# Performance work log

Hardware: AMD Instinct MI355X
Metric: run time of the kernel (lower is better)

Reference implementation:

```python
import jax, jax.numpy as jnp
import numpy as np

B, N, C = 8, 1024, 768
H, D = 12, 64
SCALE = D ** -0.5
EPS = 1e-5

def layernorm(x, g, b):
    mu = jnp.mean(x, axis=-1, keepdims=True)
    var = jnp.var(x, axis=-1, keepdims=True)
    return (x - mu) * jax.lax.rsqrt(var + EPS) * g + b

def setup_inputs() -> dict:
    key = jax.random.key(0)
    ks = jax.random.split(key, 5)
    return {
        "x": jax.random.normal(ks[0], (B, N, C), jnp.float32),
        "qkv_w": jax.random.normal(ks[1], (3 * C, C), jnp.float32) * 0.02,
        "qkv_b": jax.random.normal(ks[2], (3 * C,), jnp.float32) * 0.02,
        "qn_g": jnp.ones((D,), jnp.float32),
        "qn_b": jnp.zeros((D,), jnp.float32),
        "kn_g": jnp.ones((D,), jnp.float32),
        "kn_b": jnp.zeros((D,), jnp.float32),
        "proj_w": jax.random.normal(ks[3], (C, C), jnp.float32) * 0.02,
        "proj_b": jnp.zeros((C,), jnp.float32),
    }

def reference(x, qkv_w, qkv_b, qn_g, qn_b, kn_g, kn_b, proj_w, proj_b):
    # qkv projection: [B,N,3C] -> [3,B,H,N,D]
    qkv = jnp.einsum('bnc,oc->bno', x, qkv_w) + qkv_b
    qkv = qkv.reshape(B, N, 3, H, D).transpose(2, 0, 3, 1, 4)
    q, k, v = qkv[0], qkv[1], qkv[2]
    q = layernorm(q, qn_g, qn_b) * SCALE
    k = layernorm(k, kn_g, kn_b)
    # explicit attention matrix [B,H,N,N] (module stores it)
    attn = jax.nn.softmax(jnp.einsum('bhqd,bhkd->bhqk', q, k), axis=-1)
    out = jnp.einsum('bhqk,bhkd->bhqd', attn, v)
    out = out.transpose(0, 2, 1, 3).reshape(B, N, C)
    out = jnp.einsum('bnc,oc->bno', out, proj_w) + proj_b
    return out
```

## Files before the change

### kernel.cpp

```cpp
#include <hip/hip_runtime.h>
#include <cstdint>

#define Bz 8
#define Nn 1024
#define Cc 768
#define Hh 12
#define Dd 64
#define C3 2304
#define BN 8192

constexpr float EPS = 1e-5f;
constexpr float QSCALE = 0.125f * 1.44269504088896340736f;

typedef __attribute__((ext_vector_type(8))) short bf16x8;
typedef _Float16 f16x8 __attribute__((ext_vector_type(8)));
typedef __attribute__((ext_vector_type(4))) float f32x4;
typedef __attribute__((ext_vector_type(16))) float f32x16;

__device__ __forceinline__ short f2b(float f) {
    union { float f; unsigned u; } x; x.f = f;
    unsigned r = x.u + 0x7FFFu + ((x.u >> 16) & 1u);
    return (short)(r >> 16);
}
__device__ __forceinline__ unsigned cvtpk(float a, float b) {
    unsigned r;
    asm("v_cvt_pk_bf16_f32 %0, %1, %2" : "=v"(r) : "v"(a), "v"(b));
    return r;
}

__device__ __forceinline__ f32x4 MFMAH(f16x8 a, f16x8 b, f32x4 c) {
    return __builtin_amdgcn_mfma_f32_16x16x32_f16(a, b, c, 0, 0, 0);
}
__device__ __forceinline__ f32x16 MFMA32(bf16x8 a, bf16x8 b, f32x16 c) {
    return __builtin_amdgcn_mfma_f32_32x32x16_bf16(a, b, c, 0, 0, 0);
}
__device__ __forceinline__ f16x8 ldf16(const _Float16* p) { return *(const f16x8*)p; }
__device__ __forceinline__ void gld16(const void* g, void* l) {
    __builtin_amdgcn_global_load_lds((const __attribute__((address_space(1))) unsigned int*)g,
                                     (__attribute__((address_space(3))) unsigned int*)(l),
                                     16, 0, 0);
}

__global__ __launch_bounds__(256) void cvt_all(
    const float* __restrict__ x, const float* __restrict__ wq, const float* __restrict__ wp,
    _Float16* __restrict__ xh, _Float16* __restrict__ wqh, _Float16* __restrict__ wph)
{
    const int n1 = BN * Cc / 8, n2 = n1 + C3 * Cc / 8, n3 = n2 + Cc * Cc / 8;
    int i = blockIdx.x * 256 + threadIdx.x;
    const float* s; _Float16* d; int off;
    if (i < n1)      { s = x;  d = xh;  off = i; }
    else if (i < n2) { s = wq; d = wqh; off = i - n1; }
    else if (i < n3) { s = wp; d = wph; off = i - n2; }
    else return;
    float4 a = *(const float4*)(s + (size_t)off * 8);
    float4 b = *(const float4*)(s + (size_t)off * 8 + 4);
    f16x8 o;
    o[0] = (_Float16)a.x; o[1] = (_Float16)a.y; o[2] = (_Float16)a.z; o[3] = (_Float16)a.w;
    o[4] = (_Float16)b.x; o[5] = (_Float16)b.y; o[6] = (_Float16)b.z; o[7] = (_Float16)b.w;
    *(f16x8*)(d + (size_t)off * 8) = o;
}

template<int EPI>
__global__ __launch_bounds__(256, 4) void gemm_f16(
    const _Float16* __restrict__ A,
    const _Float16* __restrict__ W,
    const float* __restrict__ bias,
    float* __restrict__ Out,
    short* __restrict__ qp, short* __restrict__ kp, short* __restrict__ vp,
    const float* __restrict__ qg, const float* __restrict__ qb,
    const float* __restrict__ kg, const float* __restrict__ kb,
    int nx)
{
    __shared__ _Float16 As[128 * 64];
    __shared__ _Float16 Bs[128 * 64];
    const int tid = threadIdx.x;
    const int lane = tid & 63;
    const int w = tid >> 6;
    const int wr = w >> 1, wc = w & 1;
    const int l15 = lane & 15, l4 = lane >> 4;
    const int lr = lane >> 3;
    const int lslot = lane & 7;

    const int chunk = gridDim.x >> 3;
    const int wg = (blockIdx.x & 7) * chunk + (blockIdx.x >> 3);
    const int by = wg / nx;
    int bx = wg % nx;
    if (by & 1) bx = nx - 1 - bx;
    const int m0 = by * 128;
    const int n0 = bx * 128;

    auto stage = [&](int kt) {
        const int k0 = kt * 64;
#pragma unroll
        for (int j = 0; j < 8; ++j) {
            int i = w * 8 + j;
            int isA = (i < 16);
            int ib = isA ? i : i - 16;
            int row = ib * 8 + lr;
            int gslot = lslot ^ (row & 7);
            const _Float16* src = (isA ? A + (size_t)(m0 + row) * 768
                                       : W + (size_t)(n0 + row) * 768) + k0 + gslot * 8;
            _Float16* dst = (isA ? As : Bs) + ib * 512;
            gld16(src, dst);
        }
    };

    f32x4 acc[4][4];
#pragma unroll
    for (int mi = 0; mi < 4; ++mi)
#pragma unroll
        for (int ni = 0; ni < 4; ++ni) { acc[mi][ni][0]=0.f; acc[mi][ni][1]=0.f; acc[mi][ni][2]=0.f; acc[mi][ni][3]=0.f; }

    stage(0);
    for (int kt = 0; kt < 12; ++kt) {
        __syncthreads();
#pragma unroll
        for (int ks = 0; ks < 2; ++ks) {
            f16x8 af[4], bfr[4];
#pragma unroll
            for (int mi = 0; mi < 4; ++mi) {
                int row = wr * 64 + mi * 16 + l15;
                int slot = (ks * 4 + l4) ^ (row & 7);
                af[mi] = ldf16(&As[row * 64 + slot * 8]);
            }
#pragma unroll
            for (int ni = 0; ni < 4; ++ni) {
                int row = wc * 64 + ni * 16 + l15;
                int slot = (ks * 4 + l4) ^ (row & 7);
                bfr[ni] = ldf16(&Bs[row * 64 + slot * 8]);
            }
#pragma unroll
            for (int mi = 0; mi < 4; ++mi)
#pragma unroll
                for (int ni = 0; ni < 4; ++ni)
                    acc[mi][ni] = MFMAH(af[mi], bfr[ni], acc[mi][ni]);
        }
        __syncthreads();
        if (kt < 11) stage(kt + 1);
    }

    if (EPI == 0) {
#pragma unroll
        for (int mi = 0; mi < 4; ++mi)
#pragma unroll
            for (int r = 0; r < 4; ++r) {
                int row = m0 + wr * 64 + mi * 16 + l4 * 4 + r;
#pragma unroll
                for (int ni = 0; ni < 4; ++ni) {
                    int col = n0 + wc * 64 + ni * 16 + l15;
                    Out[(size_t)row * Cc + col] = acc[mi][ni][r] + bias[col];
                }
            }
    } else {
        const int ncol0 = n0 + wc * 64;
        const int type = ncol0 / Cc;
        const int h = (ncol0 % Cc) >> 6;
        const float* gptr = (type == 0) ? qg : kg;
        const float* bptr = (type == 0) ? qb : kb;
        float biasv[4], gv[4], bv[4];
#pragma unroll
        for (int ni = 0; ni < 4; ++ni) {
            int d = ni * 16 + l15;
            biasv[ni] = bias[ncol0 + d];
            if (type < 2) { gv[ni] = gptr[d]; bv[ni] = bptr[d]; }
        }
        short* plane = (type == 0) ? qp : (type == 1) ? kp : vp;
#pragma unroll
        for (int mi = 0; mi < 4; ++mi)
#pragma unroll
            for (int r = 0; r < 4; ++r) {
                float v[4];
#pragma unroll
                for (int ni = 0; ni < 4; ++ni) v[ni] = acc[mi][ni][r] + biasv[ni];
                int row = m0 + wr * 64 + mi * 16 + l4 * 4 + r;
                size_t base = ((size_t)row * Hh + h) * 64;
                if (type < 2) {
                    float s = v[0] + v[1] + v[2] + v[3];
#pragma unroll
                    for (int off = 1; off < 16; off <<= 1) s += __shfl_xor(s, off);
                    float mu = s * (1.0f / 64.0f);
                    float s2 = 0.f;
#pragma unroll
                    for (int ni = 0; ni < 4; ++ni) { float dv = v[ni] - mu; s2 += dv * dv; }
#pragma unroll
                    for (int off = 1; off < 16; off <<= 1) s2 += __shfl_xor(s2, off);
                    float inv = rsqrtf(s2 * (1.0f / 64.0f) + EPS);
#pragma unroll
                    for (int ni = 0; ni < 4; ++ni) {
                        float rr = (v[ni] - mu) * inv * gv[ni] + bv[ni];
                        if (type == 0) rr *= QSCALE;
                        plane[base + ni * 16 + l15] = f2b(rr);
                    }
                } else {
#pragma unroll
                    for (int ni = 0; ni < 4; ++ni)
                        plane[base + ni * 16 + l15] = f2b(v[ni]);
                }
            }
    }
}

__global__ __launch_bounds__(128, 3) void flash_attn_mfma(
    const short* __restrict__ qp, const short* __restrict__ kp, const short* __restrict__ vp,
    _Float16* __restrict__ att)
{
    __shared__ short kls[64 * 64];
    __shared__ short vtl[2][64 * 64];
    const int tid = threadIdx.x;
    const int lane = tid & 63;
    const int w = tid >> 6;
    const int l31 = lane & 31;
    const int hi = lane >> 5;
    const int lr = lane >> 3;
    const int lslot = lane & 7;
    const int bid = (blockIdx.x & 7) * 192 + (blockIdx.x >> 3);
    const int qt = bid & 15;
    const int bh = bid >> 4;
    const int h = bh % Hh;
    const int b = bh / Hh;
    const int q0 = qt * 64;
    const size_t hbase = ((size_t)b * Nn * Hh + h) * 64;
    const int n0v = (tid & 31) * 2, d0v = (tid >> 5) * 16;
    const int khalf = n0v & 31;
    const int t2v = n0v >> 5;
    const int ksig = khalf ^ ((((khalf >> 2) ^ (khalf >> 3)) & 1) * 12);
    const int colv = t2v * 32 + ksig;

    bf16x8 qf[4];
    {
        const short* qsrc = qp + hbase + (size_t)(q0 + w * 32 + l31) * 768 + hi * 8;
#pragma unroll
        for (int ds = 0; ds < 4; ++ds)
            qf[ds] = *(const bf16x8*)(qsrc + ds * 16);
    }

    auto kstage = [&](int kt) {
#pragma unroll
        for (int j = 0; j < 4; ++j) {
            int i = w * 4 + j;
            int row = i * 8 + lr;
            gld16(kp + hbase + (size_t)(kt * 64 + row) * 768 + (lslot ^ lr) * 8,
                  &kls[i * 512]);
        }
    };
    auto vload = [&](int kt, bf16x8* va) {
        const short* s0 = vp + hbase + (size_t)(kt * 64 + n0v) * 768 + d0v;
        va[0] = *(const bf16x8*)s0;
        va[1] = *(const bf16x8*)(s0 + 8);
        va[2] = *(const bf16x8*)(s0 + 768);
        va[3] = *(const bf16x8*)(s0 + 768 + 8);
    };
    auto vcommit = [&](int buf, const bf16x8* va) {
#pragma unroll
        for (int g = 0; g < 2; ++g)
#pragma unroll
            for (int j = 0; j < 8; ++j) {
                int d = d0v + g * 8 + j;
                int fv = (d ^ (d >> 3)) & 7;
                unsigned pku = (unsigned short)va[g][j] | ((unsigned)(unsigned short)va[g + 2][j] << 16);
                *(unsigned*)&vtl[buf][d * 64 + (((colv >> 3) ^ fv) << 3) + (colv & 7)] = pku;
            }
    };

    kstage(0);
    {
        bf16x8 va[4];
        vload(0, va);
        vcommit(0, va);
    }
    __syncthreads();

    f32x16 o0, o1;
#pragma unroll
    for (int i = 0; i < 16; ++i) { o0[i] = 0.f; o1[i] = 0.f; }
    float lrun = 0.f;

    for (int kt = 0; kt < 16; ++kt) {
        const int cur = kt & 1, nxt = cur ^ 1;
        bf16x8 va[4];
        if (kt < 15) vload(kt + 1, va);
        f32x16 st0, st1;
#pragma unroll
        for (int i = 0; i < 16; ++i) { st0[i] = 0.f; st1[i] = 0.f; }
        __builtin_amdgcn_s_setprio(1);
#pragma unroll
        for (int ds = 0; ds < 4; ++ds) {
            bf16x8 kf0 = *(const bf16x8*)&kls[l31 * 64 + (((ds * 2 + hi) ^ (l31 & 7)) << 3)];
            bf16x8 kf1 = *(const bf16x8*)&kls[(32 + l31) * 64 + (((ds * 2 + hi) ^ ((32 + l31) & 7)) << 3)];
            st0 = MFMA32(kf0, qf[ds], st0);
            st1 = MFMA32(kf1, qf[ds], st1);
        }
        __builtin_amdgcn_s_setprio(0);
        __builtin_amdgcn_s_barrier();
        if (kt < 15) kstage(kt + 1);
        unsigned pk[2][8];
#pragma unroll
        for (int i = 0; i < 16; ++i) st0[i] = exp2f(st0[i]);
#pragma unroll
        for (int i = 0; i < 16; ++i) st1[i] = exp2f(st1[i]);
        {
            float a0 = 0.f, a1 = 0.f;
#pragma unroll
            for (int i = 0; i < 16; ++i) { a0 += st0[i]; a1 += st1[i]; }
            lrun += a0 + a1;
        }
#pragma unroll
        for (int i = 0; i < 8; ++i) { pk[0][i] = cvtpk(st0[2 * i], st0[2 * i + 1]);
                                      pk[1][i] = cvtpk(st1[2 * i], st1[2 * i + 1]); }
        __builtin_amdgcn_s_setprio(1);
#pragma unroll
        for (int t2 = 0; t2 < 2; ++t2)
#pragma unroll
            for (int c = 0; c < 2; ++c) {
                union { bf16x8 v; unsigned u[4]; } a;
                a.u[0] = pk[t2][c * 4 + 0]; a.u[1] = pk[t2][c * 4 + 1];
                a.u[2] = pk[t2][c * 4 + 2]; a.u[3] = pk[t2][c * 4 + 3];
#pragma unroll
                for (int nt = 0; nt < 2; ++nt) {
                    int r = nt * 32 + l31;
                    int fv = (r ^ (r >> 3)) & 7;
                    bf16x8 vf = *(const bf16x8*)&vtl[cur][r * 64 + (((t2 * 4 + c * 2 + hi) ^ fv) << 3)];
                    if (nt == 0) o0 = MFMA32(a.v, vf, o0);
                    else         o1 = MFMA32(a.v, vf, o1);
                }
            }
        __builtin_amdgcn_s_setprio(0);
        if (kt < 15) vcommit(nxt, va);
        __syncthreads();
    }

    lrun += __shfl_xor(lrun, 32);
    float linv = 1.0f / lrun;
#pragma unroll
    for (int r = 0; r < 16; ++r) {
        int qr = (r & 3) + 8 * (r >> 2) + 4 * hi;
        float invr = __shfl(linv, qr);
        int row = q0 + w * 32 + qr;
        _Float16* dst = att + (size_t)(b * Nn + row) * Cc + h * 64 + l31;
        dst[0]  = (_Float16)(o0[r] * invr);
        dst[32] = (_Float16)(o1[r] * invr);
    }
}

extern "C" void kernel_launch(void* const* d_in, const int* in_sizes, int n_in,
                              void* d_out, int out_size, void* d_ws, size_t ws_size,
                              hipStream_t stream)
{
    const float* x      = (const float*)d_in[0];
    const float* qkv_w  = (const float*)d_in[1];
    const float* qkv_b  = (const float*)d_in[2];
    const float* qn_g   = (const float*)d_in[3];
    const float* qn_b   = (const float*)d_in[4];
    const float* kn_g   = (const float*)d_in[5];
    const float* kn_b   = (const float*)d_in[6];
    const float* proj_w = (const float*)d_in[7];
    const float* proj_b = (const float*)d_in[8];
    float* out = (float*)d_out;

    char* ws = (char*)d_ws;
    short*    qp  = (short*)(ws);
    short*    kp  = (short*)(ws + 12582912);
    short*    vp  = (short*)(ws + 25165824);
    _Float16* att = (_Float16*)(ws + 37748736);
    _Float16* xh  = (_Float16*)(ws + 50331648);
    _Float16* wqh = (_Float16*)(ws + 62914560);
    _Float16* wph = (_Float16*)(ws + 66453504);

    {
        const int n3 = BN * Cc / 8 + C3 * Cc / 8 + Cc * Cc / 8;
        cvt_all<<<(n3 + 255) / 256, 256, 0, stream>>>(x, qkv_w, proj_w, xh, wqh, wph);
    }
    gemm_f16<1><<<(BN / 128) * (C3 / 128), 256, 0, stream>>>(
        xh, wqh, qkv_b, nullptr, qp, kp, vp, qn_g, qn_b, kn_g, kn_b, C3 / 128);
    flash_attn_mfma<<<Bz * Hh * 16, 128, 0, stream>>>(qp, kp, vp, att);
    gemm_f16<0><<<(BN / 128) * (Cc / 128), 256, 0, stream>>>(
        att, wph, proj_b, out, nullptr, nullptr, nullptr, nullptr, nullptr, nullptr, nullptr, Cc / 128);
}
```

Before: 126.8 us.

## Double query tile per attention block and double-buffer K in shared memory

Each attention block now handles 128 query rows (64 per wave, two 32-row halves) instead of 64, so every K/V tile loaded into LDS is reused across twice as many queries and the grid halves. The K tile gets a second LDS buffer so the next tile is prefetched at the top of the iteration, which removes the mid-loop barrier. The V transpose packing uses a byte-permute intrinsic instead of shift/or. The cost is more accumulator registers and lower occupancy (launch bound 2 instead of 3), with fewer blocks to spread across CUs.

```diff
diff --git a/kernel.cpp b/kernel.cpp
--- a/kernel.cpp
+++ b/kernel.cpp
@@ -200,11 +200,11 @@
     }
 }
 
-__global__ __launch_bounds__(128, 3) void flash_attn_mfma(
+__global__ __launch_bounds__(128, 2) void flash_attn_mfma(
     const short* __restrict__ qp, const short* __restrict__ kp, const short* __restrict__ vp,
     _Float16* __restrict__ att)
 {
-    __shared__ short kls[64 * 64];
+    __shared__ short kls[2][64 * 64];
     __shared__ short vtl[2][64 * 64];
     const int tid = threadIdx.x;
     const int lane = tid & 63;
@@ -213,12 +213,12 @@
     const int hi = lane >> 5;
     const int lr = lane >> 3;
     const int lslot = lane & 7;
-    const int bid = (blockIdx.x & 7) * 192 + (blockIdx.x >> 3);
-    const int qt = bid & 15;
-    const int bh = bid >> 4;
+    const int bid = (blockIdx.x & 7) * 96 + (blockIdx.x >> 3);
+    const int qt = bid & 7;
+    const int bh = bid >> 3;
     const int h = bh % Hh;
     const int b = bh / Hh;
-    const int q0 = qt * 64;
+    const int q0 = qt * 128;
     const size_t hbase = ((size_t)b * Nn * Hh + h) * 64;
     const int n0v = (tid & 31) * 2, d0v = (tid >> 5) * 16;
     const int khalf = n0v & 31;
@@ -226,21 +226,22 @@
     const int ksig = khalf ^ ((((khalf >> 2) ^ (khalf >> 3)) & 1) * 12);
     const int colv = t2v * 32 + ksig;
 
-    bf16x8 qf[4];
-    {
-        const short* qsrc = qp + hbase + (size_t)(q0 + w * 32 + l31) * 768 + hi * 8;
+    bf16x8 qf[2][4];
+#pragma unroll
+    for (int qh = 0; qh < 2; ++qh) {
+        const short* qsrc = qp + hbase + (size_t)(q0 + w * 64 + qh * 32 + l31) * 768 + hi * 8;
 #pragma unroll
         for (int ds = 0; ds < 4; ++ds)
-            qf[ds] = *(const bf16x8*)(qsrc + ds * 16);
-    }
-
-    auto kstage = [&](int kt) {
+            qf[qh][ds] = *(const bf16x8*)(qsrc + ds * 16);
+    }
+
+    auto kstage = [&](int kt, int buf) {
 #pragma unroll
         for (int j = 0; j < 4; ++j) {
             int i = w * 4 + j;
             int row = i * 8 + lr;
             gld16(kp + hbase + (size_t)(kt * 64 + row) * 768 + (lslot ^ lr) * 8,
-                  &kls[i * 512]);
+                  &kls[buf][i * 512]);
         }
     };
     auto vload = [&](int kt, bf16x8* va) {
@@ -251,18 +252,22 @@
         va[3] = *(const bf16x8*)(s0 + 768 + 8);
     };
     auto vcommit = [&](int buf, const bf16x8* va) {
-#pragma unroll
-        for (int g = 0; g < 2; ++g)
+        union { bf16x8 v; unsigned u[4]; } a0, a1;
+#pragma unroll
+        for (int g = 0; g < 2; ++g) {
+            a0.v = va[g]; a1.v = va[g + 2];
 #pragma unroll
             for (int j = 0; j < 8; ++j) {
                 int d = d0v + g * 8 + j;
                 int fv = (d ^ (d >> 3)) & 7;
-                unsigned pku = (unsigned short)va[g][j] | ((unsigned)(unsigned short)va[g + 2][j] << 16);
+                unsigned pku = __builtin_amdgcn_perm(a1.u[j >> 1], a0.u[j >> 1],
+                                                     (j & 1) ? 0x07060302u : 0x05040100u);
                 *(unsigned*)&vtl[buf][d * 64 + (((colv >> 3) ^ fv) << 3) + (colv & 7)] = pku;
             }
+        }
     };
 
-    kstage(0);
+    kstage(0, 0);
     {
         bf16x8 va[4];
         vload(0, va);
@@ -270,58 +275,73 @@
     }
     __syncthreads();
 
-    f32x16 o0, o1;
-#pragma unroll
-    for (int i = 0; i < 16; ++i) { o0[i] = 0.f; o1[i] = 0.f; }
-    float lrun = 0.f;
+    f32x16 o[2][2];
+#pragma unroll
+    for (int qh = 0; qh < 2; ++qh)
+#pragma unroll
+        for (int nt = 0; nt < 2; ++nt)
+#pragma unroll
+            for (int i = 0; i < 16; ++i) o[qh][nt][i] = 0.f;
+    float lrun[2] = {0.f, 0.f};
 
     for (int kt = 0; kt < 16; ++kt) {
         const int cur = kt & 1, nxt = cur ^ 1;
         bf16x8 va[4];
-        if (kt < 15) vload(kt + 1, va);
-        f32x16 st0, st1;
-#pragma unroll
-        for (int i = 0; i < 16; ++i) { st0[i] = 0.f; st1[i] = 0.f; }
+        if (kt < 15) {
+            vload(kt + 1, va);
+            kstage(kt + 1, nxt);
+        }
+        unsigned pk[2][2][8];
+#pragma unroll
+        for (int t2 = 0; t2 < 2; ++t2) {
+            const int row = t2 * 32 + l31;
+            const int rsw = row & 7;
+            bf16x8 kf[4];
+#pragma unroll
+            for (int ds = 0; ds < 4; ++ds)
+                kf[ds] = *(const bf16x8*)&kls[cur][row * 64 + (((ds * 2 + hi) ^ rsw) << 3)];
+            f32x16 st0, st1;
+#pragma unroll
+            for (int i = 0; i < 16; ++i) { st0[i] = 0.f; st1[i] = 0.f; }
+            __builtin_amdgcn_s_setprio(1);
+#pragma unroll
+            for (int ds = 0; ds < 4; ++ds) {
+                st0 = MFMA32(kf[ds], qf[0][ds], st0);
+                st1 = MFMA32(kf[ds], qf[1][ds], st1);
+            }
+            __builtin_amdgcn_s_setprio(0);
+#pragma unroll
+            for (int i = 0; i < 16; ++i) st0[i] = exp2f(st0[i]);
+#pragma unroll
+            for (int i = 0; i < 16; ++i) st1[i] = exp2f(st1[i]);
+            {
+                float a0 = 0.f, a1 = 0.f;
+#pragma unroll
+                for (int i = 0; i < 16; ++i) { a0 += st0[i]; a1 += st1[i]; }
+                lrun[0] += a0; lrun[1] += a1;
+            }
+#pragma unroll
+            for (int i = 0; i < 8; ++i) {
+                pk[0][t2][i] = cvtpk(st0[2 * i], st0[2 * i + 1]);
+                pk[1][t2][i] = cvtpk(st1[2 * i], st1[2 * i + 1]);
+            }
+        }
         __builtin_amdgcn_s_setprio(1);
 #pragma unroll
-        for (int ds = 0; ds < 4; ++ds) {
-            bf16x8 kf0 = *(const bf16x8*)&kls[l31 * 64 + (((ds * 2 + hi) ^ (l31 & 7)) << 3)];
-            bf16x8 kf1 = *(const bf16x8*)&kls[(32 + l31) * 64 + (((ds * 2 + hi) ^ ((32 + l31) & 7)) << 3)];
-            st0 = MFMA32(kf0, qf[ds], st0);
-            st1 = MFMA32(kf1, qf[ds], st1);
-        }
-        __builtin_amdgcn_s_setprio(0);
-        __builtin_amdgcn_s_barrier();
-        if (kt < 15) kstage(kt + 1);
-        unsigned pk[2][8];
-#pragma unroll
-        for (int i = 0; i < 16; ++i) st0[i] = exp2f(st0[i]);
-#pragma unroll
-        for (int i = 0; i < 16; ++i) st1[i] = exp2f(st1[i]);
-        {
-            float a0 = 0.f, a1 = 0.f;
-#pragma unroll
-            for (int i = 0; i < 16; ++i) { a0 += st0[i]; a1 += st1[i]; }
-            lrun += a0 + a1;
-        }
-#pragma unroll
-        for (int i = 0; i < 8; ++i) { pk[0][i] = cvtpk(st0[2 * i], st0[2 * i + 1]);
-                                      pk[1][i] = cvtpk(st1[2 * i], st1[2 * i + 1]); }
-        __builtin_amdgcn_s_setprio(1);
-#pragma unroll
         for (int t2 = 0; t2 < 2; ++t2)
 #pragma unroll
             for (int c = 0; c < 2; ++c) {
-                union { bf16x8 v; unsigned u[4]; } a;
-                a.u[0] = pk[t2][c * 4 + 0]; a.u[1] = pk[t2][c * 4 + 1];
-                a.u[2] = pk[t2][c * 4 + 2]; a.u[3] = pk[t2][c * 4 + 3];
+                union { bf16x8 v; unsigned u[4]; } a0, a1;
+#pragma unroll
+                for (int q = 0; q < 4; ++q) { a0.u[q] = pk[0][t2][c * 4 + q];
+                                              a1.u[q] = pk[1][t2][c * 4 + q]; }
 #pragma unroll
                 for (int nt = 0; nt < 2; ++nt) {
                     int r = nt * 32 + l31;
                     int fv = (r ^ (r >> 3)) & 7;
                     bf16x8 vf = *(const bf16x8*)&vtl[cur][r * 64 + (((t2 * 4 + c * 2 + hi) ^ fv) << 3)];
-                    if (nt == 0) o0 = MFMA32(a.v, vf, o0);
-                    else         o1 = MFMA32(a.v, vf, o1);
+                    o[0][nt] = MFMA32(a0.v, vf, o[0][nt]);
+                    o[1][nt] = MFMA32(a1.v, vf, o[1][nt]);
                 }
             }
         __builtin_amdgcn_s_setprio(0);
@@ -329,16 +349,19 @@
         __syncthreads();
     }
 
-    lrun += __shfl_xor(lrun, 32);
-    float linv = 1.0f / lrun;
-#pragma unroll
-    for (int r = 0; r < 16; ++r) {
-        int qr = (r & 3) + 8 * (r >> 2) + 4 * hi;
-        float invr = __shfl(linv, qr);
-        int row = q0 + w * 32 + qr;
-        _Float16* dst = att + (size_t)(b * Nn + row) * Cc + h * 64 + l31;
-        dst[0]  = (_Float16)(o0[r] * invr);
-        dst[32] = (_Float16)(o1[r] * invr);
+#pragma unroll
+    for (int qh = 0; qh < 2; ++qh) {
+        float t = lrun[qh] + __shfl_xor(lrun[qh], 32);
+        float linv = 1.0f / t;
+#pragma unroll
+        for (int r = 0; r < 16; ++r) {
+            int qr = (r & 3) + 8 * (r >> 2) + 4 * hi;
+            float invr = __shfl(linv, qr);
+            int row = q0 + w * 64 + qh * 32 + qr;
+            _Float16* dst = att + (size_t)(b * Nn + row) * Cc + h * 64 + l31;
+            dst[0]  = (_Float16)(o[qh][0][r] * invr);
+            dst[32] = (_Float16)(o[qh][1][r] * invr);
+        }
     }
 }
 
@@ -372,7 +395,7 @@
     }
     gemm_f16<1><<<(BN / 128) * (C3 / 128), 256, 0, stream>>>(
         xh, wqh, qkv_b, nullptr, qp, kp, vp, qn_g, qn_b, kn_g, kn_b, C3 / 128);
-    flash_attn_mfma<<<Bz * Hh * 16, 128, 0, stream>>>(qp, kp, vp, att);
+    flash_attn_mfma<<<Bz * Hh * 8, 128, 0, stream>>>(qp, kp, vp, att);
     gemm_f16<0><<<(BN / 128) * (Cc / 128), 256, 0, stream>>>(
         att, wph, proj_b, out, nullptr, nullptr, nullptr, nullptr, nullptr, nullptr, nullptr, Cc / 128);
 }
```

Result: slower. 150.9 us (+19.0%).
